# Kernel optimization log

Measured on AMD Instinct MI355X. Metric: run time of the kernel, lower is better.

## Reference

```python
import jax, jax.numpy as jnp
import numpy as np

EMBED_DIM = 1024
NUM_HEADS = 16
PROJ_DIM = EMBED_DIM // NUM_HEADS


def setup_inputs() -> dict:
    key = jax.random.key(0)
    ks = jax.random.split(key, 11)
    B, S, D = 2, 2048, EMBED_DIM
    scale = 1.0 / np.sqrt(D)
    inp = {
        'q': jax.random.normal(ks[0], (B, S, D), jnp.float32),
        'k': jax.random.normal(ks[1], (B, S, D), jnp.float32),
        'v': jax.random.normal(ks[2], (B, S, D), jnp.float32),
        'Wq': jax.random.normal(ks[3], (D, D), jnp.float32) * scale,
        'bq': jnp.zeros((D,), jnp.float32),
        'Wk': jax.random.normal(ks[4], (D, D), jnp.float32) * scale,
        'bk': jnp.zeros((D,), jnp.float32),
        'Wv': jax.random.normal(ks[5], (D, D), jnp.float32) * scale,
        'bv': jnp.zeros((D,), jnp.float32),
        'Wo': jax.random.normal(ks[6], (D, D), jnp.float32) * scale,
        'bo': jnp.zeros((D,), jnp.float32),
        'use_causal_mask': 1,
    }
    return inp


def _split_heads(x, B):
    # [B, S, D] -> [B, H, S, Pd]
    return x.reshape(B, -1, NUM_HEADS, PROJ_DIM).transpose(0, 2, 1, 3)


def reference(q, k, v, Wq, bq, Wk, bk, Wv, bv, Wo, bo, use_causal_mask):
    B, S, D = q.shape
    qh = _split_heads(q @ Wq + bq, B)
    kh = _split_heads(k @ Wk + bk, B)
    vh = _split_heads(v @ Wv + bv, B)
    # scaled dot-product attention; scores [B, H, S, S]
    logits = jnp.einsum('bhqd,bhkd->bhqk', qh, kh) / jnp.sqrt(
        jnp.asarray(PROJ_DIM, jnp.float32))
    if use_causal_mask:
        # faithful to source: logits += log(tril * 1e-9 + 1e-9)
        tril = jnp.tril(jnp.ones((S, S), dtype=logits.dtype))
        logits = logits + jnp.log(tril * 1e-9 + 1e-9)
    attn = jax.nn.softmax(logits, axis=-1)
    out = jnp.einsum('bhqk,bhkd->bhqd', attn, vh)
    out = out.transpose(0, 2, 1, 3).reshape(B, S, D)
    return out @ Wo + bo
```

## Files before the change

### kernel.cpp

```cpp
#include <hip/hip_runtime.h>
#include <hip/hip_bf16.h>
#include <stdint.h>

#define EMBED 1024
#define NH    16
#define PD    64
#define BATCH 2
#define SEQ   2048

typedef unsigned short u16;
typedef __attribute__((ext_vector_type(8))) short bf16x8;
typedef __attribute__((ext_vector_type(4))) float f32x4;

#define WAITALL() __builtin_amdgcn_s_waitcnt(0)

__device__ __forceinline__ float b2f(u16 x) {
  unsigned u = ((unsigned)x) << 16;
  return __builtin_bit_cast(float, u);
}
__device__ __forceinline__ u16 cvtb(float x) {
  __bf16 h = (__bf16)x;
  return __builtin_bit_cast(u16, h);
}
__device__ __forceinline__ float loadIn(const void* p, size_t i, int isf32) {
  return isf32 ? ((const float*)p)[i] : b2f(((const u16*)p)[i]);
}
__device__ __forceinline__ void async16(const void* g, void* l) {
  __builtin_amdgcn_global_load_lds((const __attribute__((address_space(1))) void*)g,
                                   (__attribute__((address_space(3))) void*)l,
                                   16, 0, 0);
}

__global__ __launch_bounds__(256) void conv_qkv(const void* q, const void* k,
                                                const void* v, u16* qb, u16* kb,
                                                u16* vb, int* flag) {
  unsigned w0 = ((const unsigned*)q)[threadIdx.x & 63];
  unsigned e = (w0 >> 7) & 0xffu;
  int pred = (e >= 110 && e <= 135);
  unsigned long long m = __ballot(pred);
  const int isf32 = (__popcll(m) < 32) ? 1 : 0;
  if (blockIdx.x == 0 && blockIdx.y == 0 && threadIdx.x == 0) flag[0] = isf32;

  size_t i = ((size_t)blockIdx.x * 256 + threadIdx.x) * 8;
  const void* src = (blockIdx.y == 0) ? q : (blockIdx.y == 1) ? k : v;
  u16* dst = (blockIdx.y == 0) ? qb : (blockIdx.y == 1) ? kb : vb;
  u16 tmp[8];
  if (isf32) {
    const float* s = (const float*)src + i;
    float4 a = *(const float4*)s;
    float4 b = *(const float4*)(s + 4);
    tmp[0] = cvtb(a.x); tmp[1] = cvtb(a.y); tmp[2] = cvtb(a.z); tmp[3] = cvtb(a.w);
    tmp[4] = cvtb(b.x); tmp[5] = cvtb(b.y); tmp[6] = cvtb(b.z); tmp[7] = cvtb(b.w);
  } else {
    const uint4 r = *(const uint4*)((const u16*)src + i);
    *(uint4*)tmp = r;
  }
  *(uint4*)(dst + i) = *(uint4*)tmp;
}

__global__ __launch_bounds__(256) void conv_w(const void* Wq, const void* Wk,
                                              const void* Wv, const void* Wo,
                                              u16* out, const int* flag) {
  const int isf32 = flag[0];
  const void* W = (blockIdx.z == 0) ? Wq : (blockIdx.z == 1) ? Wk
                : (blockIdx.z == 2) ? Wv : Wo;
  u16* WT = out + (size_t)blockIdx.z * EMBED * EMBED;
  __shared__ float sh[64][65];
  int r0 = blockIdx.y * 64, c0 = blockIdx.x * 64;
  int col = threadIdx.x & 63;
  int rb  = threadIdx.x >> 6;
#pragma unroll
  for (int i = 0; i < 16; i++) {
    int row = i * 4 + rb;
    sh[row][col] = loadIn(W, (size_t)(r0 + row) * EMBED + c0 + col, isf32);
  }
  __syncthreads();
#pragma unroll
  for (int i = 0; i < 16; i++) {
    int row = i * 4 + rb;
    WT[(size_t)(c0 + row) * EMBED + r0 + col] = cvtb(sh[col][row]);
  }
}

__device__ __forceinline__ void gemm_stage(const u16* __restrict__ A,
                                           const u16* __restrict__ Bt,
                                           int tm, int tn, int kt,
                                           u16* As, u16* Bs, int tid) {
#pragma unroll
  for (int i = 0; i < 4; i++) {
    int c = i * 256 + tid;
    int row = c >> 3;
    int col = ((c & 7) << 3) ^ ((row & 7) << 3);
    async16(A + (size_t)(tm + row) * EMBED + kt + col, As + c * 8);
    async16(Bt + (size_t)(tn + row) * EMBED + kt + col, Bs + c * 8);
  }
}

__device__ __forceinline__ void gemm_compute(const u16* As, const u16* Bs,
                                             int wm, int wn, int l15, int quad,
                                             int rbx, f32x4 acc[4][4]) {
#pragma unroll
  for (int ks = 0; ks < 64; ks += 32) {
    int ko = (ks + quad * 8) ^ rbx;
    bf16x8 af[4], bf[4];
#pragma unroll
    for (int mt = 0; mt < 4; mt++)
      af[mt] = *(const bf16x8*)(As + (wm + mt * 16 + l15) * 64 + ko);
#pragma unroll
    for (int nt = 0; nt < 4; nt++)
      bf[nt] = *(const bf16x8*)(Bs + (wn + nt * 16 + l15) * 64 + ko);
#pragma unroll
    for (int mt = 0; mt < 4; mt++)
#pragma unroll
      for (int nt = 0; nt < 4; nt++)
        acc[mt][nt] = __builtin_amdgcn_mfma_f32_16x16x32_bf16(
            af[mt], bf[nt], acc[mt][nt], 0, 0, 0);
  }
}

__global__ __launch_bounds__(256) void qkv_gemm(
    const u16* qb, const u16* kb, const u16* vb, const u16* wts,
    const void* bq, const void* bk, const void* bv,
    u16* Qh, u16* Kh, u16* Vt, const int* flag) {
  __shared__ __align__(16) u16 lds[2 * 128 * 64];
  const int isf32 = flag[0];
  int z = blockIdx.z;
  const u16* A = (z == 0) ? qb : (z == 1) ? kb : vb;
  const u16* Bt = wts + (size_t)z * EMBED * EMBED;
  const void* bias = (z == 0) ? bq : (z == 1) ? bk : bv;
  int tm = blockIdx.y * 128, tn = blockIdx.x * 128;

  const int tid = threadIdx.x, lane = tid & 63, wv = tid >> 6;
  const int wm = (wv >> 1) * 64, wn = (wv & 1) * 64;
  const int l15 = lane & 15, quad = lane >> 4;
  const int rbx = (lane & 7) << 3;
  f32x4 acc[4][4];
  f32x4 zz = {0.f, 0.f, 0.f, 0.f};
#pragma unroll
  for (int i = 0; i < 4; i++)
#pragma unroll
    for (int j = 0; j < 4; j++) acc[i][j] = zz;

  for (int kt = 0; kt < EMBED; kt += 64) {
    gemm_stage(A, Bt, tm, tn, kt, lds, lds + 8192, tid);
    WAITALL();
    __syncthreads();
    gemm_compute(lds, lds + 8192, wm, wn, l15, quad, rbx, acc);
    __syncthreads();
  }

  int rbase = tm + wm + (quad << 2);
  int cbase = tn + wn + l15;
  if (z < 2) {
    u16* dst = (z == 0) ? Qh : Kh;
#pragma unroll
    for (int mt = 0; mt < 4; mt++)
#pragma unroll
      for (int nt = 0; nt < 4; nt++) {
        int col = cbase + nt * 16;
        float bv_ = loadIn(bias, col, isf32);
        int h = col >> 6, p = col & 63;
#pragma unroll
        for (int j = 0; j < 4; j++) {
          int row = rbase + mt * 16 + j;
          int b = row >> 11, s = row & 2047;
          dst[(((size_t)(b * NH + h) * SEQ) + s) * PD + p] =
              cvtb(acc[mt][nt][j] + bv_);
        }
      }
  } else {
#pragma unroll
    for (int mt = 0; mt < 4; mt++)
#pragma unroll
      for (int nt = 0; nt < 4; nt++) {
        int col = cbase + nt * 16;
        float bv_ = loadIn(bias, col, isf32);
        int h = col >> 6, p = col & 63;
        int row0 = rbase + mt * 16;
        int b = row0 >> 11, s0 = row0 & 2047;
        int beta = s0 >> 5, w = s0 & 31;
        int pos = (beta << 5) + (((w >> 2) & 3) << 3) + ((w >> 4) << 2);
        ushort4 pk;
        pk.x = cvtb(acc[mt][nt][0] + bv_);
        pk.y = cvtb(acc[mt][nt][1] + bv_);
        pk.z = cvtb(acc[mt][nt][2] + bv_);
        pk.w = cvtb(acc[mt][nt][3] + bv_);
        *(ushort4*)(Vt + ((size_t)(b * NH + h) * PD + p) * SEQ + pos) = pk;
      }
  }
}

__global__ __launch_bounds__(256, 4) void attn(const u16* __restrict__ Qh,
                                               const u16* __restrict__ Kh,
                                               const u16* __restrict__ Vt,
                                               u16* __restrict__ O,
                                               const int* __restrict__ maskflag) {
  __shared__ __align__(16) u16 sh[4 * 64 * 64];
  u16* const Ksb0 = sh;
  u16* const Ksb1 = sh + 4096;
  u16* const Vsb0 = sh + 8192;
  u16* const Vsb1 = sh + 12288;
  u16* const Qs   = Ksb1;
  const int bh = blockIdx.y;
  const int qt = blockIdx.x * 64;
  const int tid = threadIdx.x, lane = tid & 63, wv = tid >> 6;
  const int l15 = lane & 15, quad = lane >> 4;
  const int rbx = (lane & 7) << 3;
  const size_t head = (size_t)bh * SEQ * PD;
  const bool causal = (maskflag[0] != 0);
  const float C = 0.18033688011112042f;

  const int c0 = tid, c1 = 256 + tid;
  const int r0 = c0 >> 3, r1 = c1 >> 3;
  const int x0 = ((c0 & 7) << 3) ^ ((r0 & 7) << 3);
  const int x1 = ((c1 & 7) << 3) ^ ((r1 & 7) << 3);

  async16(Qh + head + (size_t)(qt + r0) * PD + x0, Qs + c0 * 8);
  async16(Qh + head + (size_t)(qt + r1) * PD + x1, Qs + c1 * 8);
  async16(Kh + head + (size_t)r0 * PD + x0, Ksb0 + c0 * 8);
  async16(Kh + head + (size_t)r1 * PD + x1, Ksb0 + c1 * 8);
  async16(Vt + head + (size_t)r0 * SEQ + x0, Vsb0 + c0 * 8);
  async16(Vt + head + (size_t)r1 * SEQ + x1, Vsb0 + c1 * 8);
  WAITALL();
  __syncthreads();

  bf16x8 qf[2];
#pragma unroll
  for (int ks = 0; ks < 2; ks++) {
    int ko = (ks * 32 + quad * 8) ^ rbx;
    qf[ks] = *(const bf16x8*)(Qs + (wv * 16 + l15) * 64 + ko);
  }
  __syncthreads();

  float lacc = 0.f;
  f32x4 oacc[4];
  f32x4 z4 = {0.f, 0.f, 0.f, 0.f};
#pragma unroll
  for (int mt = 0; mt < 4; mt++) oacc[mt] = z4;

  const int rowq = qt + wv * 16;
  const int qrow = rowq + l15;

  for (int t = 0; t < SEQ / 64; t++) {
    const int k0 = t * 64;
    const int cur = t & 1;
    if (t + 1 < SEQ / 64) {
      const int kn = k0 + 64;
      u16* Kn = cur ? Ksb0 : Ksb1;
      u16* Vn = cur ? Vsb0 : Vsb1;
      async16(Kh + head + (size_t)(kn + r0) * PD + x0, Kn + c0 * 8);
      async16(Kh + head + (size_t)(kn + r1) * PD + x1, Kn + c1 * 8);
      async16(Vt + head + (size_t)r0 * SEQ + kn + x0, Vn + c0 * 8);
      async16(Vt + head + (size_t)r1 * SEQ + kn + x1, Vn + c1 * 8);
    }
    const u16* Ksc = cur ? Ksb1 : Ksb0;
    const u16* Vsc = cur ? Vsb1 : Vsb0;

    f32x4 st[4];
#pragma unroll
    for (int kt = 0; kt < 4; kt++) st[kt] = z4;
    __builtin_amdgcn_s_setprio(1);
#pragma unroll
    for (int ks = 0; ks < 2; ks++) {
      int ko = (ks * 32 + quad * 8) ^ rbx;
#pragma unroll
      for (int kt = 0; kt < 4; kt++) {
        bf16x8 kf = *(const bf16x8*)(Ksc + (kt * 16 + l15) * 64 + ko);
        st[kt] = __builtin_amdgcn_mfma_f32_16x16x32_bf16(kf, qf[ks], st[kt], 0, 0, 0);
      }
    }
    __builtin_amdgcn_s_setprio(0);

    const int mode = !causal ? 0 : (k0 > qt + 63 ? 2 : (k0 + 63 <= qt ? 0 : 1));
    const float ub = (mode == 2) ? -17.f : -16.f;
    unsigned pw[2][4];
#pragma unroll
    for (int kt = 0; kt < 4; kt++) {
      float p[4];
#pragma unroll
      for (int r = 0; r < 4; r++) {
        float bias = ub;
        if (mode == 1) {
          int kappa = k0 + kt * 16 + 4 * quad + r;
          bias = (kappa > qrow) ? -17.f : -16.f;
        }
        p[r] = exp2f(fmaf(st[kt][r], C, bias));
      }
      lacc += (p[0] + p[1]) + (p[2] + p[3]);
      pw[kt >> 1][(kt & 1) * 2 + 0] =
          (unsigned)cvtb(p[0]) | ((unsigned)cvtb(p[1]) << 16);
      pw[kt >> 1][(kt & 1) * 2 + 1] =
          (unsigned)cvtb(p[2]) | ((unsigned)cvtb(p[3]) << 16);
    }

    __builtin_amdgcn_s_setprio(1);
#pragma unroll
    for (int p = 0; p < 2; p++) {
      bf16x8 pf = __builtin_bit_cast(bf16x8,
          (uint4){pw[p][0], pw[p][1], pw[p][2], pw[p][3]});
#pragma unroll
      for (int mt = 0; mt < 4; mt++) {
        int row = mt * 16 + l15;
        int chunk = ((p << 2) + quad) ^ (row & 7);
        bf16x8 vf = *(const bf16x8*)(Vsc + row * 64 + (chunk << 3));
        oacc[mt] = __builtin_amdgcn_mfma_f32_16x16x32_bf16(vf, pf, oacc[mt], 0, 0, 0);
      }
    }
    __builtin_amdgcn_s_setprio(0);
    WAITALL();
    __syncthreads();
  }

  lacc += __shfl_xor(lacc, 16, 64);
  lacc += __shfl_xor(lacc, 32, 64);
  float inv = 1.f / lacc;

  const int b = bh >> 4, h = bh & 15;
#pragma unroll
  for (int mt = 0; mt < 4; mt++) {
    ushort4 w;
    w.x = cvtb(oacc[mt][0] * inv);
    w.y = cvtb(oacc[mt][1] * inv);
    w.z = cvtb(oacc[mt][2] * inv);
    w.w = cvtb(oacc[mt][3] * inv);
    *(ushort4*)(O + ((size_t)b * SEQ + qrow) * EMBED + h * PD + mt * 16 +
                4 * quad) = w;
  }
}

__global__ __launch_bounds__(256) void out_gemm(const u16* __restrict__ Ob,
                                                const u16* __restrict__ WoT,
                                                const void* __restrict__ bo,
                                                void* __restrict__ out,
                                                const int* __restrict__ flag) {
  __shared__ __align__(16) u16 lds[4 * 128 * 64];
  const int isf32 = flag[0];
  int tm = blockIdx.y * 128, tn = blockIdx.x * 128;
  const int tid = threadIdx.x, lane = tid & 63, wv = tid >> 6;
  const int wm = (wv >> 1) * 64, wn = (wv & 1) * 64;
  const int l15 = lane & 15, quad = lane >> 4;
  const int rbx = (lane & 7) << 3;
  f32x4 acc[4][4];
  f32x4 zz = {0.f, 0.f, 0.f, 0.f};
#pragma unroll
  for (int i = 0; i < 4; i++)
#pragma unroll
    for (int j = 0; j < 4; j++) acc[i][j] = zz;

  gemm_stage(Ob, WoT, tm, tn, 0, lds, lds + 8192, tid);
  WAITALL();
  __syncthreads();
  for (int kt = 0; kt < EMBED; kt += 64) {
    const int cur = (kt >> 6) & 1;
    u16* curb = lds + cur * 16384;
    if (kt + 64 < EMBED)
      gemm_stage(Ob, WoT, tm, tn, kt + 64, lds + (cur ^ 1) * 16384,
                 lds + (cur ^ 1) * 16384 + 8192, tid);
    gemm_compute(curb, curb + 8192, wm, wn, l15, quad, rbx, acc);
    WAITALL();
    __syncthreads();
  }

  int rbase = tm + wm + (quad << 2);
  int cbase = tn + wn + l15;
#pragma unroll
  for (int mt = 0; mt < 4; mt++)
#pragma unroll
    for (int nt = 0; nt < 4; nt++) {
      int col = cbase + nt * 16;
      float bv_ = loadIn(bo, col, isf32);
#pragma unroll
      for (int j = 0; j < 4; j++) {
        int row = rbase + mt * 16 + j;
        float val = acc[mt][nt][j] + bv_;
        size_t off = (size_t)row * EMBED + col;
        if (isf32) ((float*)out)[off] = val;
        else       ((u16*)out)[off]   = cvtb(val);
      }
    }
}

extern "C" void kernel_launch(void* const* d_in, const int* in_sizes, int n_in,
                              void* d_out, int out_size, void* d_ws, size_t ws_size,
                              hipStream_t stream) {
  const void* q  = d_in[0];
  const void* k  = d_in[1];
  const void* v  = d_in[2];
  const void* Wq = d_in[3];
  const void* bq = d_in[4];
  const void* Wk = d_in[5];
  const void* bk = d_in[6];
  const void* Wv = d_in[7];
  const void* bv = d_in[8];
  const void* Wo = d_in[9];
  const void* bo = d_in[10];
  const int* msk = (const int*)d_in[11];

  char* ws = (char*)d_ws;
  int*  flag  = (int*)ws;
  u16*  qb    = (u16*)(ws + 64);
  u16*  kb    = qb + (size_t)4194304;
  u16*  vb    = kb + (size_t)4194304;
  u16*  WT    = vb + (size_t)4194304;
  u16*  Qh    = WT + (size_t)4194304;
  u16*  Kh    = Qh + (size_t)4194304;
  u16*  Vt    = Kh + (size_t)4194304;
  u16*  Ob    = Vt + (size_t)4194304;

  conv_qkv<<<dim3(2048, 3), 256, 0, stream>>>(q, k, v, qb, kb, vb, flag);
  conv_w<<<dim3(16, 16, 4), 256, 0, stream>>>(Wq, Wk, Wv, Wo, WT, flag);
  qkv_gemm<<<dim3(8, 32, 3), 256, 0, stream>>>(qb, kb, vb, WT, bq, bk, bv,
                                               Qh, Kh, Vt, flag);
  attn<<<dim3(32, 32), 256, 0, stream>>>(Qh, Kh, Vt, Ob, msk);
  out_gemm<<<dim3(8, 32), 256, 0, stream>>>(Ob, WT + (size_t)3 * 1048576,
                                            bo, d_out, flag);
}
```

Baseline: 281.2 us.

## Fuse input and weight conversion kernels and remap attention blocks across XCDs

Merges the activation conversion and weight transpose kernels into one launch. Each kernel now detects the input dtype itself, so the workspace flag is no longer needed. The attention grid is remapped so that the query tiles of a given head are placed on the same XCD, which should improve L2 reuse of K/V. The cost is a redundant dtype check in every block and 1024 idle blocks in the fused conversion grid.

```diff
diff --git a/kernel.cpp b/kernel.cpp
--- a/kernel.cpp
+++ b/kernel.cpp
@@ -30,43 +30,46 @@
                                    (__attribute__((address_space(3))) void*)l,
                                    16, 0, 0);
 }
-
-__global__ __launch_bounds__(256) void conv_qkv(const void* q, const void* k,
-                                                const void* v, u16* qb, u16* kb,
-                                                u16* vb, int* flag) {
+__device__ __forceinline__ int detect_f32(const void* q) {
   unsigned w0 = ((const unsigned*)q)[threadIdx.x & 63];
   unsigned e = (w0 >> 7) & 0xffu;
-  int pred = (e >= 110 && e <= 135);
-  unsigned long long m = __ballot(pred);
-  const int isf32 = (__popcll(m) < 32) ? 1 : 0;
-  if (blockIdx.x == 0 && blockIdx.y == 0 && threadIdx.x == 0) flag[0] = isf32;
-
-  size_t i = ((size_t)blockIdx.x * 256 + threadIdx.x) * 8;
-  const void* src = (blockIdx.y == 0) ? q : (blockIdx.y == 1) ? k : v;
-  u16* dst = (blockIdx.y == 0) ? qb : (blockIdx.y == 1) ? kb : vb;
-  u16 tmp[8];
-  if (isf32) {
-    const float* s = (const float*)src + i;
-    float4 a = *(const float4*)s;
-    float4 b = *(const float4*)(s + 4);
-    tmp[0] = cvtb(a.x); tmp[1] = cvtb(a.y); tmp[2] = cvtb(a.z); tmp[3] = cvtb(a.w);
-    tmp[4] = cvtb(b.x); tmp[5] = cvtb(b.y); tmp[6] = cvtb(b.z); tmp[7] = cvtb(b.w);
-  } else {
-    const uint4 r = *(const uint4*)((const u16*)src + i);
-    *(uint4*)tmp = r;
-  }
-  *(uint4*)(dst + i) = *(uint4*)tmp;
-}
-
-__global__ __launch_bounds__(256) void conv_w(const void* Wq, const void* Wk,
-                                              const void* Wv, const void* Wo,
-                                              u16* out, const int* flag) {
-  const int isf32 = flag[0];
-  const void* W = (blockIdx.z == 0) ? Wq : (blockIdx.z == 1) ? Wk
-                : (blockIdx.z == 2) ? Wv : Wo;
-  u16* WT = out + (size_t)blockIdx.z * EMBED * EMBED;
+  unsigned long long m = __ballot(e >= 110 && e <= 135);
+  return (__popcll(m) < 32) ? 1 : 0;
+}
+
+__global__ __launch_bounds__(256) void conv_fused(
+    const void* q, const void* k, const void* v,
+    const void* Wq, const void* Wk, const void* Wv, const void* Wo,
+    u16* qb, u16* kb, u16* vb, u16* WT_all) {
   __shared__ float sh[64][65];
-  int r0 = blockIdx.y * 64, c0 = blockIdx.x * 64;
+  const int isf32 = detect_f32(q);
+
+  if (blockIdx.y < 3) {
+    size_t i = ((size_t)blockIdx.x * 256 + threadIdx.x) * 8;
+    const void* src = (blockIdx.y == 0) ? q : (blockIdx.y == 1) ? k : v;
+    u16* dst = (blockIdx.y == 0) ? qb : (blockIdx.y == 1) ? kb : vb;
+    u16 tmp[8];
+    if (isf32) {
+      const float* s = (const float*)src + i;
+      float4 a = *(const float4*)s;
+      float4 b = *(const float4*)(s + 4);
+      tmp[0] = cvtb(a.x); tmp[1] = cvtb(a.y); tmp[2] = cvtb(a.z); tmp[3] = cvtb(a.w);
+      tmp[4] = cvtb(b.x); tmp[5] = cvtb(b.y); tmp[6] = cvtb(b.z); tmp[7] = cvtb(b.w);
+    } else {
+      const uint4 r = *(const uint4*)((const u16*)src + i);
+      *(uint4*)tmp = r;
+    }
+    *(uint4*)(dst + i) = *(uint4*)tmp;
+    return;
+  }
+
+  if (blockIdx.x >= 1024) return;
+  const int z = blockIdx.x >> 8;
+  const int xy = blockIdx.x & 255;
+  const int bx = xy & 15, by = xy >> 4;
+  const void* W = (z == 0) ? Wq : (z == 1) ? Wk : (z == 2) ? Wv : Wo;
+  u16* WT = WT_all + (size_t)z * EMBED * EMBED;
+  int r0 = by * 64, c0 = bx * 64;
   int col = threadIdx.x & 63;
   int rb  = threadIdx.x >> 6;
 #pragma unroll
@@ -121,9 +124,9 @@
 __global__ __launch_bounds__(256) void qkv_gemm(
     const u16* qb, const u16* kb, const u16* vb, const u16* wts,
     const void* bq, const void* bk, const void* bv,
-    u16* Qh, u16* Kh, u16* Vt, const int* flag) {
+    u16* Qh, u16* Kh, u16* Vt, const void* qorig) {
   __shared__ __align__(16) u16 lds[2 * 128 * 64];
-  const int isf32 = flag[0];
+  const int isf32 = detect_f32(qorig);
   int z = blockIdx.z;
   const u16* A = (z == 0) ? qb : (z == 1) ? kb : vb;
   const u16* Bt = wts + (size_t)z * EMBED * EMBED;
@@ -201,8 +204,12 @@
   u16* const Vsb0 = sh + 8192;
   u16* const Vsb1 = sh + 12288;
   u16* const Qs   = Ksb1;
-  const int bh = blockIdx.y;
-  const int qt = blockIdx.x * 64;
+
+  const int lid = blockIdx.x + (blockIdx.y << 5);
+  const int xcd = lid & 7, j = lid >> 3;
+  const int bh = (xcd << 2) | (j & 3);
+  const int qt = (j >> 2) * 64;
+
   const int tid = threadIdx.x, lane = tid & 63, wv = tid >> 6;
   const int l15 = lane & 15, quad = lane >> 4;
   const int rbx = (lane & 7) << 3;
@@ -332,9 +339,9 @@
                                                 const u16* __restrict__ WoT,
                                                 const void* __restrict__ bo,
                                                 void* __restrict__ out,
-                                                const int* __restrict__ flag) {
+                                                const void* __restrict__ qorig) {
   __shared__ __align__(16) u16 lds[4 * 128 * 64];
-  const int isf32 = flag[0];
+  const int isf32 = detect_f32(qorig);
   int tm = blockIdx.y * 128, tn = blockIdx.x * 128;
   const int tid = threadIdx.x, lane = tid & 63, wv = tid >> 6;
   const int wm = (wv >> 1) * 64, wn = (wv & 1) * 64;
@@ -397,7 +404,6 @@
   const int* msk = (const int*)d_in[11];
 
   char* ws = (char*)d_ws;
-  int*  flag  = (int*)ws;
   u16*  qb    = (u16*)(ws + 64);
   u16*  kb    = qb + (size_t)4194304;
   u16*  vb    = kb + (size_t)4194304;
@@ -407,11 +413,11 @@
   u16*  Vt    = Kh + (size_t)4194304;
   u16*  Ob    = Vt + (size_t)4194304;
 
-  conv_qkv<<<dim3(2048, 3), 256, 0, stream>>>(q, k, v, qb, kb, vb, flag);
-  conv_w<<<dim3(16, 16, 4), 256, 0, stream>>>(Wq, Wk, Wv, Wo, WT, flag);
+  conv_fused<<<dim3(2048, 4), 256, 0, stream>>>(q, k, v, Wq, Wk, Wv, Wo,
+                                                qb, kb, vb, WT);
   qkv_gemm<<<dim3(8, 32, 3), 256, 0, stream>>>(qb, kb, vb, WT, bq, bk, bv,
-                                               Qh, Kh, Vt, flag);
+                                               Qh, Kh, Vt, q);
   attn<<<dim3(32, 32), 256, 0, stream>>>(Qh, Kh, Vt, Ob, msk);
   out_gemm<<<dim3(8, 32), 256, 0, stream>>>(Ob, WT + (size_t)3 * 1048576,
-                                            bo, d_out, flag);
-}
+                                            bo, d_out, q);
+}
```

Result: no change. 276.2 us (-1.8%).
